# Kernel optimization log

Measured on AMD Instinct MI355X. Metric: run time of the kernel, lower is better.

Reference implementation:

```python
import jax, jax.numpy as jnp
import numpy as np

TILE = 16            # TILE_WIDTH == TILE_HEIGHT in the Taichi kernel
H, W = 512, 512
TV, TU = H // TILE, W // TILE
NT = TV * TU         # number of 16x16 tiles
PPT = 64             # depth-sorted points assigned to each tile (uniform/padded)
N = NT * PPT


def setup_inputs() -> dict:
    key = jax.random.key(0)
    ks = jax.random.split(key, 7)
    # each tile owns a contiguous depth-sorted chunk of the global point list
    tile_of_point = jnp.arange(N) // PPT
    tu = (tile_of_point % TU).astype(jnp.float32)
    tv = (tile_of_point // TU).astype(jnp.float32)
    center = jnp.stack([tu * TILE + TILE / 2, tv * TILE + TILE / 2], -1)
    point_uv = center + jax.random.normal(ks[0], (N, 2)) * 6.0
    # conic = inverse 2x2 covariance packed as [a, b, c]; keep positive definite
    a = jax.random.uniform(ks[1], (N,), minval=0.02, maxval=0.3)
    c = jax.random.uniform(ks[2], (N,), minval=0.02, maxval=0.3)
    b = jax.random.uniform(ks[3], (N,), minval=-0.5, maxval=0.5) * jnp.sqrt(a * c)
    point_uv_conic = jnp.stack([a, b, c], -1)
    point_alpha_after_activation = jax.random.uniform(ks[4], (N,))
    point_color = jax.random.uniform(ks[5], (N, 3))
    # depths sorted within each tile chunk (front-to-back order, as after radix sort)
    point_depth = jnp.sort(
        jax.random.uniform(ks[6], (N,), minval=0.5, maxval=50.0).reshape(NT, PPT), axis=-1
    ).reshape(N)
    tile_point_indices = jnp.arange(N, dtype=jnp.int32).reshape(NT, PPT)
    return dict(point_uv=point_uv, point_uv_conic=point_uv_conic,
                point_alpha_after_activation=point_alpha_after_activation,
                point_color=point_color, point_depth=point_depth,
                tile_point_indices=tile_point_indices,
                camera_height=H, camera_width=W)


def _to_image(x, tv, tu):
    # x: [NT, TILE*TILE, ...] -> [H, W, ...] (tiles row-major, pixels row-major in tile)
    rest = x.shape[2:]
    x = x.reshape(tv, tu, TILE, TILE, *rest)
    x = jnp.swapaxes(x, 1, 2)
    return x.reshape(tv * TILE, tu * TILE, *rest)


def reference(point_uv, point_uv_conic, point_alpha_after_activation, point_color,
              point_depth, tile_point_indices, camera_height, camera_width):
    TU_ = camera_width // TILE
    TV_ = camera_height // TILE
    NT_ = TU_ * TV_
    PPT_ = tile_point_indices.shape[1]
    # gather per-tile point attributes: [NT, PPT, ...]
    g_uv = point_uv[tile_point_indices]
    g_conic = point_uv_conic[tile_point_indices]
    g_alpha = point_alpha_after_activation[tile_point_indices]
    g_color = point_color[tile_point_indices]
    g_depth = point_depth[tile_point_indices]
    # pixel centers for every tile: [NT, 256]
    p = jnp.arange(TILE * TILE)
    tid = jnp.arange(NT_)
    pix_u = (tid % TU_)[:, None].astype(jnp.float32) * TILE + (p % TILE).astype(jnp.float32)[None, :] + 0.5
    pix_v = (tid // TU_)[:, None].astype(jnp.float32) * TILE + (p // TILE).astype(jnp.float32)[None, :] + 0.5
    # Gaussian density from conic: exp(-0.5*(a dx^2 + c dy^2) - b dx dy)  [NT, 256, PPT]
    dx = pix_u[:, :, None] - g_uv[:, None, :, 0]
    dy = pix_v[:, :, None] - g_uv[:, None, :, 1]
    ca = g_conic[:, None, :, 0]; cb = g_conic[:, None, :, 1]; cc = g_conic[:, None, :, 2]
    dens = jnp.exp(-0.5 * (ca * dx * dx + cc * dy * dy) - cb * dx * dy)
    alpha = dens * g_alpha[:, None, :]
    visible = alpha >= 1.0 / 255.0           # kernel: continue if alpha < 1/255
    alpha_c = jnp.where(visible, jnp.minimum(alpha, 0.99), 0.0)
    one_m = 1.0 - alpha_c
    cp = jnp.cumprod(one_m, axis=-1)
    Ti = jnp.concatenate([jnp.ones_like(cp[..., :1]), cp[..., :-1]], axis=-1)  # exclusive transmittance
    # point whose next_T < 1e-4 saturates the pixel and is itself skipped
    trigger = visible & (Ti * one_m < 1e-4)
    saturated = jnp.cumsum(trigger.astype(jnp.int32), axis=-1) > 0
    contributes = visible & ~saturated
    w = jnp.where(contributes, alpha_c * Ti, 0.0)   # per-point compositing weight
    acc_color = jnp.einsum('tpk,tkc->tpc', w, g_color)
    norm = jnp.sum(w, axis=-1)
    acc_depth = jnp.sum(w * g_depth[:, None, :], axis=-1)
    T_final = jnp.prod(jnp.where(contributes, one_m, 1.0), axis=-1)
    valid_count = jnp.sum(contributes, axis=-1).astype(jnp.int32)
    j = jnp.arange(PPT_, dtype=jnp.int32)
    last = jnp.max(jnp.where(contributes, j[None, None, :] + 1, 0), axis=-1)
    last_offset = (jnp.arange(NT_, dtype=jnp.int32) * PPT_)[:, None] + last
    rasterized_image = _to_image(acc_color, TV_, TU_)
    rasterized_depth = _to_image(acc_depth / jnp.maximum(norm, 1e-6), TV_, TU_)
    pixel_accumulated_alpha = _to_image(1.0 - T_final, TV_, TU_)
    pixel_offset_of_last_effective_point = _to_image(last_offset, TV_, TU_)
    pixel_valid_point_count = _to_image(valid_count, TV_, TU_)
    return (rasterized_image, rasterized_depth, pixel_accumulated_alpha,
            pixel_offset_of_last_effective_point, pixel_valid_point_count)
```

## Files before the change

kernel.cpp:

```cpp
#include <hip/hip_runtime.h>
#include <hip/hip_fp16.h>

#define TILE 16
#define PPT 64

#if __has_builtin(__builtin_amdgcn_exp2f)
#define EXP2F(x) __builtin_amdgcn_exp2f(x)
#else
#define EXP2F(x) exp2f(x)
#endif

__device__ __forceinline__ int read_dim(const int* p) {
    int v = *p;
    if (v >= TILE && v <= 65536 && (v % TILE) == 0) return v;
    float f = __int_as_float(v);
    return (int)f;
}

__global__ __launch_bounds__(256, 4) void gsplat_raster_kernel(
    const float* __restrict__ point_uv,
    const float* __restrict__ point_conic,
    const float* __restrict__ point_alpha,
    const float* __restrict__ point_color,
    const float* __restrict__ point_depth,
    const int*   __restrict__ tile_point_indices,
    const int*   __restrict__ cam_h_p,
    const int*   __restrict__ cam_w_p,
    float* __restrict__ out)
{
    const int t = blockIdx.x;
    const int p = threadIdx.x;

    const int W  = read_dim(cam_w_p);
    const int H  = read_dim(cam_h_p);
    const int TU = W / TILE;
    const int n_pix = H * W;

    __shared__ float4 sA[PPT];
    __shared__ float4 sB[PPT];

    const float L2E = 1.4426950408889634f;
    if (p < PPT) {
        const int gi = tile_point_indices[t * PPT + p];
        const float2 uv = ((const float2*)point_uv)[gi];
        const float ca = point_conic[gi * 3 + 0];
        const float cc = point_conic[gi * 3 + 2];
        sA[p] = make_float4(uv.x, uv.y, -0.5f * L2E * ca, -0.5f * L2E * cc);
    } else if (p < 2 * PPT) {
        const int q  = p - PPT;
        const int gi = tile_point_indices[t * PPT + q];
        const float cb = point_conic[gi * 3 + 1];
        const float al = point_alpha[gi];
        const __half2 rg = __floats2half2_rn(point_color[gi * 3 + 0],
                                             point_color[gi * 3 + 1]);
        const __half2 bd = __floats2half2_rn(point_color[gi * 3 + 2],
                                             point_depth[gi]);
        sB[q] = make_float4(-L2E * cb, __log2f(al),
                            __builtin_bit_cast(float, rg),
                            __builtin_bit_cast(float, bd));
    }
    __syncthreads();

    const int tu = t % TU;
    const int tv = t / TU;
    const int pu = p % TILE;
    const int pv = p / TILE;
    const float pix_u = (float)(tu * TILE + pu) + 0.5f;
    const float pix_v = (float)(tv * TILE + pv) + 0.5f;

    float T = 1.0f;
    float accr = 0.0f, accg = 0.0f, accb = 0.0f;
    float accd = 0.0f, norm = 0.0f;
    int count = 0, last = 0;
    bool sat = false;

    for (int c8 = 0; c8 < PPT / 8; ++c8) {
        #pragma unroll
        for (int k = 0; k < 8; ++k) {
            const int j = c8 * 8 + k;
            const float4 A = sA[j];
            const float4 B = sB[j];

            const float dx = pix_u - A.x;
            const float dy = pix_v - A.y;
            const float e = fmaf(fmaf(A.z, dx, B.x * dy), dx,
                                 fmaf(A.w * dy, dy, B.y));
            const float alpha = EXP2F(e);

            const bool  vis     = alpha >= (1.0f / 255.0f);
            const float alpha_c = fminf(alpha, 0.99f);
            const float one_m   = 1.0f - alpha_c;
            const float Tone    = T * one_m;
            const bool  ntrig   = Tone >= 1e-4f;
            const bool  contrib = vis && ntrig && !sat;
            sat = sat || (vis && !ntrig);

            const float w = contrib ? alpha_c * T : 0.0f;
            const __half2 rg = __builtin_bit_cast(__half2, B.z);
            const __half2 bd = __builtin_bit_cast(__half2, B.w);
            accr = fmaf(w, __low2float(rg),  accr);
            accg = fmaf(w, __high2float(rg), accg);
            accb = fmaf(w, __low2float(bd),  accb);
            accd = fmaf(w, __high2float(bd), accd);
            norm += w;
            count += contrib;
            last = contrib ? j + 1 : last;
            T = contrib ? Tone : T;
        }
        if (__all(sat)) break;
    }

    const int r = tv * TILE + pv;
    const int c = tu * TILE + pu;
    const int pix = r * W + c;

    out[pix * 3 + 0] = accr;
    out[pix * 3 + 1] = accg;
    out[pix * 3 + 2] = accb;
    out[n_pix * 3 + pix] = accd / fmaxf(norm, 1e-6f);
    out[n_pix * 4 + pix] = 1.0f - T;
    out[n_pix * 5 + pix] = (float)(t * PPT + last);
    out[n_pix * 6 + pix] = (float)count;
}

extern "C" void kernel_launch(void* const* d_in, const int* in_sizes, int n_in,
                              void* d_out, int out_size, void* d_ws, size_t ws_size,
                              hipStream_t stream) {
    const float* point_uv    = (const float*)d_in[0];
    const float* point_conic = (const float*)d_in[1];
    const float* point_alpha = (const float*)d_in[2];
    const float* point_color = (const float*)d_in[3];
    const float* point_depth = (const float*)d_in[4];
    const int*   tpi         = (const int*)d_in[5];
    const int*   cam_h       = (const int*)d_in[6];
    const int*   cam_w       = (const int*)d_in[7];

    const int NT = in_sizes[5] / PPT;

    gsplat_raster_kernel<<<NT, 256, 0, stream>>>(
        point_uv, point_conic, point_alpha, point_color, point_depth,
        tpi, cam_h, cam_w, (float*)d_out);
}
```

Before: 20.31 us.

## Pre-gather point records into workspace and read them directly in raster kernel

Adds a separate gather kernel that packs each tile's points into 64-byte float records in the workspace. A new raster kernel then reads those records straight from global memory, with uniform addresses across the block, instead of staging them in LDS behind a barrier. It falls back to the old LDS kernel when the workspace is too small. This removes the per-block scattered gather and the __syncthreads, but adds a second launch, an extra global write and read of the records, and loads inside the hot loop.

```diff
diff --git a/kernel.cpp b/kernel.cpp
--- a/kernel.cpp
+++ b/kernel.cpp
@@ -17,7 +17,109 @@
     return (int)f;
 }
 
-__global__ __launch_bounds__(256, 4) void gsplat_raster_kernel(
+__global__ __launch_bounds__(256) void gsplat_gather_kernel(
+    const float* __restrict__ point_uv,
+    const float* __restrict__ point_conic,
+    const float* __restrict__ point_alpha,
+    const float* __restrict__ point_color,
+    const float* __restrict__ point_depth,
+    const int*   __restrict__ tile_point_indices,
+    float* __restrict__ rec, int n)
+{
+    const int i = blockIdx.x * blockDim.x + threadIdx.x;
+    if (i >= n) return;
+    const float L2E = 1.4426950408889634f;
+    const int gi = tile_point_indices[i];
+    const float2 uv = ((const float2*)point_uv)[gi];
+    const float ca = point_conic[gi * 3 + 0];
+    const float cb = point_conic[gi * 3 + 1];
+    const float cc = point_conic[gi * 3 + 2];
+    float4* o = (float4*)(rec + (size_t)i * 16);
+    o[0] = make_float4(uv.x, uv.y, -0.5f * L2E * ca, -0.5f * L2E * cc);
+    o[1] = make_float4(-L2E * cb, __log2f(point_alpha[gi]),
+                       point_color[gi * 3 + 0], point_color[gi * 3 + 1]);
+    o[2] = make_float4(point_color[gi * 3 + 2], point_depth[gi], 0.0f, 0.0f);
+}
+
+__global__ __launch_bounds__(256, 4) void gsplat_raster_smem_kernel(
+    const float* __restrict__ rec,
+    const int*   __restrict__ cam_h_p,
+    const int*   __restrict__ cam_w_p,
+    float* __restrict__ out)
+{
+    const int t = blockIdx.x;
+    const int p = threadIdx.x;
+
+    const int W  = read_dim(cam_w_p);
+    const int H  = read_dim(cam_h_p);
+    const int TU = W / TILE;
+    const int n_pix = H * W;
+
+    const float4* __restrict__ tile_rec =
+        (const float4*)(rec + (size_t)t * PPT * 16);
+
+    const int tu = t % TU;
+    const int tv = t / TU;
+    const int pu = p % TILE;
+    const int pv = p / TILE;
+    const float pix_u = (float)(tu * TILE + pu) + 0.5f;
+    const float pix_v = (float)(tv * TILE + pv) + 0.5f;
+
+    float T = 1.0f;
+    float accr = 0.0f, accg = 0.0f, accb = 0.0f;
+    float accd = 0.0f, norm = 0.0f;
+    int count = 0, last = 0;
+    bool sat = false;
+
+    for (int c8 = 0; c8 < PPT / 8; ++c8) {
+        #pragma unroll
+        for (int k = 0; k < 8; ++k) {
+            const int j = c8 * 8 + k;
+            const float4 A = tile_rec[j * 4 + 0];
+            const float4 B = tile_rec[j * 4 + 1];
+            const float4 C = tile_rec[j * 4 + 2];
+
+            const float dx = pix_u - A.x;
+            const float dy = pix_v - A.y;
+            const float e = fmaf(fmaf(A.z, dx, B.x * dy), dx,
+                                 fmaf(A.w * dy, dy, B.y));
+            const float alpha = EXP2F(e);
+
+            const bool  vis     = alpha >= (1.0f / 255.0f);
+            const float alpha_c = fminf(alpha, 0.99f);
+            const float one_m   = 1.0f - alpha_c;
+            const float Tone    = T * one_m;
+            const bool  ntrig   = Tone >= 1e-4f;
+            const bool  contrib = vis && ntrig && !sat;
+            sat = sat || (vis && !ntrig);
+
+            const float w = contrib ? alpha_c * T : 0.0f;
+            accr = fmaf(w, B.z, accr);
+            accg = fmaf(w, B.w, accg);
+            accb = fmaf(w, C.x, accb);
+            accd = fmaf(w, C.y, accd);
+            norm += w;
+            count += contrib;
+            last = contrib ? j + 1 : last;
+            T = contrib ? Tone : T;
+        }
+        if (__all(sat)) break;
+    }
+
+    const int r = tv * TILE + pv;
+    const int c = tu * TILE + pu;
+    const int pix = r * W + c;
+
+    out[pix * 3 + 0] = accr;
+    out[pix * 3 + 1] = accg;
+    out[pix * 3 + 2] = accb;
+    out[n_pix * 3 + pix] = accd / fmaxf(norm, 1e-6f);
+    out[n_pix * 4 + pix] = 1.0f - T;
+    out[n_pix * 5 + pix] = (float)(t * PPT + last);
+    out[n_pix * 6 + pix] = (float)count;
+}
+
+__global__ __launch_bounds__(256, 4) void gsplat_raster_lds_kernel(
     const float* __restrict__ point_uv,
     const float* __restrict__ point_conic,
     const float* __restrict__ point_alpha,
@@ -43,19 +145,18 @@
     if (p < PPT) {
         const int gi = tile_point_indices[t * PPT + p];
         const float2 uv = ((const float2*)point_uv)[gi];
-        const float ca = point_conic[gi * 3 + 0];
-        const float cc = point_conic[gi * 3 + 2];
-        sA[p] = make_float4(uv.x, uv.y, -0.5f * L2E * ca, -0.5f * L2E * cc);
+        sA[p] = make_float4(uv.x, uv.y,
+                            -0.5f * L2E * point_conic[gi * 3 + 0],
+                            -0.5f * L2E * point_conic[gi * 3 + 2]);
     } else if (p < 2 * PPT) {
         const int q  = p - PPT;
         const int gi = tile_point_indices[t * PPT + q];
-        const float cb = point_conic[gi * 3 + 1];
-        const float al = point_alpha[gi];
         const __half2 rg = __floats2half2_rn(point_color[gi * 3 + 0],
                                              point_color[gi * 3 + 1]);
         const __half2 bd = __floats2half2_rn(point_color[gi * 3 + 2],
                                              point_depth[gi]);
-        sB[q] = make_float4(-L2E * cb, __log2f(al),
+        sB[q] = make_float4(-L2E * point_conic[gi * 3 + 1],
+                            __log2f(point_alpha[gi]),
                             __builtin_bit_cast(float, rg),
                             __builtin_bit_cast(float, bd));
     }
@@ -135,9 +236,20 @@
     const int*   cam_h       = (const int*)d_in[6];
     const int*   cam_w       = (const int*)d_in[7];
 
-    const int NT = in_sizes[5] / PPT;
-
-    gsplat_raster_kernel<<<NT, 256, 0, stream>>>(
-        point_uv, point_conic, point_alpha, point_color, point_depth,
-        tpi, cam_h, cam_w, (float*)d_out);
-}
+    const int n_pts = in_sizes[5];
+    const int NT    = n_pts / PPT;
+    const size_t need = (size_t)n_pts * 64;
+
+    if (ws_size >= need) {
+        float* rec = (float*)d_ws;
+        gsplat_gather_kernel<<<(n_pts + 255) / 256, 256, 0, stream>>>(
+            point_uv, point_conic, point_alpha, point_color, point_depth,
+            tpi, rec, n_pts);
+        gsplat_raster_smem_kernel<<<NT, 256, 0, stream>>>(
+            rec, cam_h, cam_w, (float*)d_out);
+    } else {
+        gsplat_raster_lds_kernel<<<NT, 256, 0, stream>>>(
+            point_uv, point_conic, point_alpha, point_color, point_depth,
+            tpi, cam_h, cam_w, (float*)d_out);
+    }
+}
```

Measured after the change: 29.78 us. +46.6%, slower.
